# Performance work log

Hardware: AMD Instinct MI355X
Metric: run time of the kernel (lower is better)

## Reference

```python
import jax, jax.numpy as jnp
import numpy as np

N = 100000          # number of nodes (queries == sources here)
DEG = 32            # uniform neighbor count
E = N * DEG         # total edges
C_IN = 8
HID = 32
C_OUT = 32


def setup_inputs() -> dict:
    key = jax.random.key(0)
    k1, k2, k3, k4, k5 = jax.random.split(key, 5)
    in_features = jax.random.normal(k1, (N, C_IN), dtype=jnp.float32)
    in_weights = jax.random.uniform(k2, (N,), dtype=jnp.float32)
    # MLP: Linear(2*C_IN -> HID), GELU, Linear(HID -> C_OUT)
    W1 = jax.random.normal(k3, (2 * C_IN, HID), dtype=jnp.float32) / np.sqrt(2 * C_IN)
    b1 = jnp.zeros((HID,), dtype=jnp.float32)
    W2 = jax.random.normal(k4, (HID, C_OUT), dtype=jnp.float32) / np.sqrt(HID)
    b2 = jnp.zeros((C_OUT,), dtype=jnp.float32)
    neighbor_index = jax.random.randint(k5, (E,), 0, N, dtype=jnp.int64)
    row_splits = (jnp.arange(N + 1, dtype=jnp.int64) * DEG)  # uniform CSR splits
    return {"in_features": in_features, "in_weights": in_weights,
            "W1": W1, "b1": b1, "W2": W2, "b2": b2,
            "neighbor_index": neighbor_index, "row_splits": row_splits}


def reference(in_features, in_weights, W1, b1, W2, b2, neighbor_index, row_splits):
    num_edges = neighbor_index.shape[0]
    num_out = row_splits.shape[0] - 1  # M output nodes
    # segment id of each edge (== repeat_interleave of node ids by row counts)
    seg = jnp.searchsorted(row_splits, jnp.arange(num_edges), side="right") - 1
    gathered = in_features[neighbor_index]          # [E, C_in] neighbor gather
    self_feats = in_features[seg]                   # [E, C_in] repeated self features
    agg = jnp.concatenate([gathered, self_feats], axis=1)  # [E, 2*C_in]
    h = jax.nn.gelu(agg @ W1 + b1)                  # [E, HID]
    h = h @ W2 + b2                                 # [E, C_out]
    h = in_weights[neighbor_index][:, None] * h     # quadrature weighting
    sums = jax.ops.segment_sum(h, seg, num_segments=num_out)  # segment_csr sum
    counts = (row_splits[1:] - row_splits[:-1]).astype(h.dtype)
    out = sums / jnp.maximum(counts, 1)[:, None]    # reduce='mean'
    return out
```

## Files before the change

kernel.cpp:

```cpp
#include <hip/hip_runtime.h>

#define DEG 32
#define HID 32
#define CIN 8

typedef float v2f __attribute__((ext_vector_type(2)));
typedef short bf16x8 __attribute__((ext_vector_type(8)));
typedef float f32x16 __attribute__((ext_vector_type(16)));

#define GELU_A ((float)(2.0 * 1.4426950408889634 * 0.7978845608028654))
#define GELU_B ((float)(2.0 * 1.4426950408889634 * 0.7978845608028654 * 0.044715))

__device__ __forceinline__ unsigned f2bf(float f) {
    unsigned b = __float_as_uint(f);
    return (b + 0x7fffu + ((b >> 16) & 1u)) >> 16;
}
__device__ __forceinline__ unsigned pack2(float lo, float hi) {
    return f2bf(lo) | (f2bf(hi) << 16);
}

__global__ __launch_bounds__(256) void precompute_xw(
    const float* __restrict__ x, const float* __restrict__ W1,
    const float* __restrict__ W2, unsigned* __restrict__ x16,
    unsigned* __restrict__ w1f, unsigned* __restrict__ w2f, int N) {
    int tid = blockIdx.x * 256 + threadIdx.x;
    if (blockIdx.x == 0) {
        int t = threadIdx.x;
        if (t < 64) {
            int kb = (t >> 5) * 8, col = t & 31;
            uint4 o;
            o.x = pack2(W1[(kb + 0) * HID + col], W1[(kb + 1) * HID + col]);
            o.y = pack2(W1[(kb + 2) * HID + col], W1[(kb + 3) * HID + col]);
            o.z = pack2(W1[(kb + 4) * HID + col], W1[(kb + 5) * HID + col]);
            o.w = pack2(W1[(kb + 6) * HID + col], W1[(kb + 7) * HID + col]);
            *(uint4*)(w1f + t * 4) = o;
        } else if (t < 192) {
            int u = t - 64;
            int f = u >> 6, l = u & 63;
            int kb = f * 16 + ((l >> 5) * 8), col = l & 31;
            uint4 o;
            o.x = pack2(W2[(kb + 0) * HID + col], W2[(kb + 1) * HID + col]);
            o.y = pack2(W2[(kb + 2) * HID + col], W2[(kb + 3) * HID + col]);
            o.z = pack2(W2[(kb + 4) * HID + col], W2[(kb + 5) * HID + col]);
            o.w = pack2(W2[(kb + 6) * HID + col], W2[(kb + 7) * HID + col]);
            *(uint4*)(w2f + (f * 64 + l) * 4) = o;
        }
    }
    if (tid < N) {
        const float4* xp = (const float4*)(x + (size_t)tid * CIN);
        float4 a = xp[0], b = xp[1];
        uint4 o;
        o.x = pack2(a.x, a.y);  o.y = pack2(a.z, a.w);
        o.z = pack2(b.x, b.y);  o.w = pack2(b.z, b.w);
        *(uint4*)(x16 + (size_t)tid * 4) = o;
    }
}

__global__ __launch_bounds__(256) void git_core(
    const unsigned* __restrict__ x16, const unsigned* __restrict__ w1f,
    const float* __restrict__ wgt, const float* __restrict__ b1,
    const int* __restrict__ nbr, unsigned short* __restrict__ g16,
    float* __restrict__ wsum, int N) {
    __shared__ float sw[4 * DEG];

    int t = threadIdx.x;
    int wv = t >> 6;
    int l  = t & 63;
    int l5 = l & 31;
    int hi = l >> 5;
    int node = blockIdx.x * 4 + wv;
    int nc = node < N ? node : (N - 1);

    int   jn = nbr[nc * DEG + l5];
    float w  = wgt[jn];
    if (hi == 0) sw[wv * DEG + l5] = w;

    float ws = w;
    ws += __shfl_xor(ws, 1);  ws += __shfl_xor(ws, 2);
    ws += __shfl_xor(ws, 4);  ws += __shfl_xor(ws, 8);
    ws += __shfl_xor(ws, 16);

    int arow = hi ? nc : jn;
    bf16x8 af = *((const bf16x8*)x16 + arow);
    bf16x8 bf = *((const bf16x8*)w1f + l);
    float myb1 = b1[l5];

    f32x16 acc;
#pragma unroll
    for (int i = 0; i < 16; ++i) acc[i] = myb1;
    acc = __builtin_amdgcn_mfma_f32_32x32x16_bf16(af, bf, acc, 0, 0, 0);

    const float* swp = &sw[wv * DEG + hi * 4];
    float4 wq0 = *(const float4*)(swp);
    float4 wq1 = *(const float4*)(swp + 8);
    float4 wq2 = *(const float4*)(swp + 16);
    float4 wq3 = *(const float4*)(swp + 24);
    float wqa[16] = {wq0.x, wq0.y, wq0.z, wq0.w,  wq1.x, wq1.y, wq1.z, wq1.w,
                     wq2.x, wq2.y, wq2.z, wq2.w,  wq3.x, wq3.y, wq3.z, wq3.w};

    v2f gacc = {0.f, 0.f};
#pragma unroll
    for (int i = 0; i < 16; i += 2) {
        v2f tt = {acc[i], acc[i + 1]};
        v2f x2 = tt * tt;
        v2f zz = tt * (x2 * (-GELU_B) + (-GELU_A));
        v2f ee;
        ee.x = __builtin_amdgcn_exp2f(zz.x);  ee.y = __builtin_amdgcn_exp2f(zz.y);
        v2f dd = ee + 1.0f;
        v2f rr;
        rr.x = __builtin_amdgcn_rcpf(dd.x);   rr.y = __builtin_amdgcn_rcpf(dd.y);
        v2f wp = {wqa[i], wqa[i + 1]};
        gacc += wp * (tt * rr);
    }
    float g = gacc.x + gacc.y;
    g += __shfl_xor(g, 32);

    if (node < N && hi == 0) {
        g16[(size_t)node * HID + l5] = (unsigned short)f2bf(g);
        if (l5 == 0) wsum[node] = ws;
    }
}

__global__ __launch_bounds__(256) void epilogue_mfma(
    const unsigned short* __restrict__ g16, const unsigned* __restrict__ w2f,
    const float* __restrict__ wsum, const float* __restrict__ b2,
    float* __restrict__ out, int N) {
    int t = threadIdx.x;
    int wv = t >> 6;
    int l  = t & 63;
    int l5 = l & 31;
    int hi = l >> 5;
    int tile = blockIdx.x * 4 + wv;
    int ntiles = (N + 31) >> 5;
    if (tile >= ntiles) return;
    int nb = tile * 32;

    int row = nb + l5;  if (row >= N) row = N - 1;
    bf16x8 a1 = *(const bf16x8*)(g16 + (size_t)row * HID + hi * 8);
    bf16x8 a2 = *(const bf16x8*)(g16 + (size_t)row * HID + 16 + hi * 8);
    bf16x8 bf1 = *((const bf16x8*)w2f + l);
    bf16x8 bf2 = *((const bf16x8*)w2f + 64 + l);

    f32x16 acc = {};
    acc = __builtin_amdgcn_mfma_f32_32x32x16_bf16(a1, bf1, acc, 0, 0, 0);
    acc = __builtin_amdgcn_mfma_f32_32x32x16_bf16(a2, bf2, acc, 0, 0, 0);

    float myb2 = b2[l5];
    float wsa[16];
    if (nb + 32 <= N) {
        const float* wp = wsum + nb + hi * 4;
        float4 q0 = *(const float4*)(wp);
        float4 q1 = *(const float4*)(wp + 8);
        float4 q2 = *(const float4*)(wp + 16);
        float4 q3 = *(const float4*)(wp + 24);
        wsa[0]=q0.x; wsa[1]=q0.y; wsa[2]=q0.z; wsa[3]=q0.w;
        wsa[4]=q1.x; wsa[5]=q1.y; wsa[6]=q1.z; wsa[7]=q1.w;
        wsa[8]=q2.x; wsa[9]=q2.y; wsa[10]=q2.z; wsa[11]=q2.w;
        wsa[12]=q3.x; wsa[13]=q3.y; wsa[14]=q3.z; wsa[15]=q3.w;
    } else {
#pragma unroll
        for (int i = 0; i < 16; ++i) {
            int r = nb + (i & 3) + 8 * (i >> 2) + 4 * hi;
            wsa[i] = wsum[r < N ? r : (N - 1)];
        }
    }
#pragma unroll
    for (int i = 0; i < 16; ++i) {
        int r = nb + (i & 3) + 8 * (i >> 2) + 4 * hi;
        if (r < N)
            out[(size_t)r * HID + l5] = fmaf(wsa[i], myb2, acc[i]) * (1.0f / DEG);
    }
}

__global__ __launch_bounds__(256) void fused_fallback(
    const float* __restrict__ x, const float* __restrict__ wgt,
    const float* __restrict__ W1, const float* __restrict__ b1,
    const float* __restrict__ W2, const float* __restrict__ b2,
    const int* __restrict__ nbr, float* __restrict__ out, int N) {
    __shared__ float sW2[HID * HID];
    __shared__ float sb2[HID];
    __shared__ int2  sp[8 * DEG];
    int t = threadIdx.x;
#pragma unroll
    for (int i = 0; i < 4; ++i) sW2[t + i * 256] = W2[t + i * 256];
    if (t < HID) sb2[t] = b2[t];
    int slot = t >> 5, hid = t & 31;
    int node = blockIdx.x * 8 + slot;
    bool valid = node < N;
    int nc = valid ? node : (N - 1);
    int   j_own = nbr[nc * DEG + hid];
    float w_own = wgt[j_own];
    sp[slot * DEG + hid] = make_int2(j_own * (CIN * 4), __float_as_int(w_own));
    const float4* xip = (const float4*)(x + (size_t)nc * CIN);
    float4 xa = xip[0], xb = xip[1];
    float w1t[8];
#pragma unroll
    for (int k = 0; k < 8; ++k) w1t[k] = W1[k * HID + hid];
    float vb = b1[hid];
    vb = fmaf(xa.x, W1[ 8 * HID + hid], vb);
    vb = fmaf(xa.y, W1[ 9 * HID + hid], vb);
    vb = fmaf(xa.z, W1[10 * HID + hid], vb);
    vb = fmaf(xa.w, W1[11 * HID + hid], vb);
    vb = fmaf(xb.x, W1[12 * HID + hid], vb);
    vb = fmaf(xb.y, W1[13 * HID + hid], vb);
    vb = fmaf(xb.z, W1[14 * HID + hid], vb);
    vb = fmaf(xb.w, W1[15 * HID + hid], vb);
    float ws = w_own;
    ws += __shfl_xor(ws, 1);  ws += __shfl_xor(ws, 2);
    ws += __shfl_xor(ws, 4);  ws += __shfl_xor(ws, 8);
    ws += __shfl_xor(ws, 16);
    __syncthreads();
    const char* xbytes = (const char*)x;
    const int2* myp = &sp[slot * DEG];
    float g = 0.f;
#pragma unroll 8
    for (int e = 0; e < DEG; ++e) {
        int2  p  = myp[e];
        float wjv = __int_as_float(p.y);
        const float4* xjp = (const float4*)(xbytes + (unsigned)p.x);
        float4 a = xjp[0], b = xjp[1];
        float tin = vb;
        tin = fmaf(a.x, w1t[0], tin); tin = fmaf(a.y, w1t[1], tin);
        tin = fmaf(a.z, w1t[2], tin); tin = fmaf(a.w, w1t[3], tin);
        tin = fmaf(b.x, w1t[4], tin); tin = fmaf(b.y, w1t[5], tin);
        tin = fmaf(b.z, w1t[6], tin); tin = fmaf(b.w, w1t[7], tin);
        float x2 = tin * tin;
        float z  = tin * fmaf(GELU_B, x2, GELU_A);
        float e2 = __builtin_amdgcn_exp2f(z);
        float r  = __builtin_amdgcn_rcpf(1.0f + e2);
        g = fmaf(wjv, fmaf(-tin, r, tin), g);
    }
    float acc = 0.f;
#pragma unroll
    for (int h = 0; h < HID; ++h) {
        float gh = __shfl(g, h, 32);
        acc = fmaf(gh, sW2[h * HID + hid], acc);
    }
    if (valid) out[(size_t)node * HID + hid] = fmaf(ws, sb2[hid], acc) * (1.0f / DEG);
}

extern "C" void kernel_launch(void* const* d_in, const int* in_sizes, int n_in,
                              void* d_out, int out_size, void* d_ws, size_t ws_size,
                              hipStream_t stream) {
    const float* x   = (const float*)d_in[0];
    const float* wq  = (const float*)d_in[1];
    const float* W1  = (const float*)d_in[2];
    const float* b1  = (const float*)d_in[3];
    const float* W2  = (const float*)d_in[4];
    const float* b2  = (const float*)d_in[5];
    const int*   nbr = (const int*)d_in[6];
    float* out = (float*)d_out;

    int N = in_sizes[1];

    size_t off_x16 = 0;
    size_t off_g16 = (off_x16 + (size_t)N * 16 + 255) & ~(size_t)255;
    size_t off_ws  = (off_g16 + (size_t)N * 64 + 255) & ~(size_t)255;
    size_t off_w1  = (off_ws  + (size_t)N * 4  + 255) & ~(size_t)255;
    size_t off_w2  = off_w1 + 1024;
    size_t need    = off_w2 + 2048;

    if (ws_size >= need) {
        unsigned*       x16  = (unsigned*)((char*)d_ws + off_x16);
        unsigned short* g16p = (unsigned short*)((char*)d_ws + off_g16);
        float*          wsum = (float*)((char*)d_ws + off_ws);
        unsigned*       w1f  = (unsigned*)((char*)d_ws + off_w1);
        unsigned*       w2f  = (unsigned*)((char*)d_ws + off_w2);

        int blocks_pre = (N + 255) / 256;
        precompute_xw<<<blocks_pre, 256, 0, stream>>>(x, W1, W2, x16, w1f, w2f, N);

        int blocks_main = (N + 3) / 4;
        git_core<<<blocks_main, 256, 0, stream>>>(x16, w1f, wq, b1, nbr, g16p, wsum, N);

        int ntiles = (N + 31) / 32;
        int blocks_epi = (ntiles + 3) / 4;
        epilogue_mfma<<<blocks_epi, 256, 0, stream>>>(g16p, w2f, wsum, b2, out, N);
    } else {
        int blocks = (N + 7) / 8;
        fused_fallback<<<blocks, 256, 0, stream>>>(x, wq, W1, b1, W2, b2, nbr, out, N);
    }
}
```

Baseline: 121.4 us.

## Fuse GELU-aggregation and output MFMA into one kernel via shared memory

Merges the core kernel and the epilogue kernel into a single kernel. Each wave now handles two nodes, and each block covers eight nodes. The per-node aggregated hidden vectors and weight sums are staged in shared memory instead of a global bf16 buffer, and one wave then runs the W2 MFMA for the block. This removes a global write and read of the intermediate, plus one kernel launch. In exchange it adds a block barrier, leaves three of four waves idle during the epilogue, and wastes most rows of the 32x32 MFMA.

Result: faster. 114.3 us (-5.8%).

```diff
diff --git a/kernel.cpp b/kernel.cpp
--- a/kernel.cpp
+++ b/kernel.cpp
@@ -56,52 +56,18 @@
     }
 }
 
-__global__ __launch_bounds__(256) void git_core(
-    const unsigned* __restrict__ x16, const unsigned* __restrict__ w1f,
-    const float* __restrict__ wgt, const float* __restrict__ b1,
-    const int* __restrict__ nbr, unsigned short* __restrict__ g16,
-    float* __restrict__ wsum, int N) {
-    __shared__ float sw[4 * DEG];
-
-    int t = threadIdx.x;
-    int wv = t >> 6;
-    int l  = t & 63;
-    int l5 = l & 31;
-    int hi = l >> 5;
-    int node = blockIdx.x * 4 + wv;
-    int nc = node < N ? node : (N - 1);
-
-    int   jn = nbr[nc * DEG + l5];
-    float w  = wgt[jn];
-    if (hi == 0) sw[wv * DEG + l5] = w;
-
-    float ws = w;
-    ws += __shfl_xor(ws, 1);  ws += __shfl_xor(ws, 2);
-    ws += __shfl_xor(ws, 4);  ws += __shfl_xor(ws, 8);
-    ws += __shfl_xor(ws, 16);
-
-    int arow = hi ? nc : jn;
-    bf16x8 af = *((const bf16x8*)x16 + arow);
-    bf16x8 bf = *((const bf16x8*)w1f + l);
-    float myb1 = b1[l5];
-
-    f32x16 acc;
-#pragma unroll
-    for (int i = 0; i < 16; ++i) acc[i] = myb1;
-    acc = __builtin_amdgcn_mfma_f32_32x32x16_bf16(af, bf, acc, 0, 0, 0);
-
-    const float* swp = &sw[wv * DEG + hi * 4];
+__device__ __forceinline__ float gelu_reduce(const f32x16& acc, const float* swp,
+                                             float b1v) {
     float4 wq0 = *(const float4*)(swp);
     float4 wq1 = *(const float4*)(swp + 8);
     float4 wq2 = *(const float4*)(swp + 16);
     float4 wq3 = *(const float4*)(swp + 24);
     float wqa[16] = {wq0.x, wq0.y, wq0.z, wq0.w,  wq1.x, wq1.y, wq1.z, wq1.w,
                      wq2.x, wq2.y, wq2.z, wq2.w,  wq3.x, wq3.y, wq3.z, wq3.w};
-
     v2f gacc = {0.f, 0.f};
 #pragma unroll
     for (int i = 0; i < 16; i += 2) {
-        v2f tt = {acc[i], acc[i + 1]};
+        v2f tt = {acc[i] + b1v, acc[i + 1] + b1v};
         v2f x2 = tt * tt;
         v2f zz = tt * (x2 * (-GELU_B) + (-GELU_A));
         v2f ee;
@@ -114,61 +80,90 @@
     }
     float g = gacc.x + gacc.y;
     g += __shfl_xor(g, 32);
-
-    if (node < N && hi == 0) {
-        g16[(size_t)node * HID + l5] = (unsigned short)f2bf(g);
-        if (l5 == 0) wsum[node] = ws;
-    }
-}
-
-__global__ __launch_bounds__(256) void epilogue_mfma(
-    const unsigned short* __restrict__ g16, const unsigned* __restrict__ w2f,
-    const float* __restrict__ wsum, const float* __restrict__ b2,
-    float* __restrict__ out, int N) {
+    return g;
+}
+
+__global__ __launch_bounds__(256, 5) void git_fused(
+    const unsigned* __restrict__ x16, const unsigned* __restrict__ w1f,
+    const unsigned* __restrict__ w2f, const float* __restrict__ wgt,
+    const float* __restrict__ b1, const float* __restrict__ b2,
+    const int* __restrict__ nbr, float* __restrict__ out, int N) {
+    __shared__ float          sw[8 * DEG];
+    __shared__ unsigned short sg[32 * 40];
+    __shared__ float          sws[32];
+
     int t = threadIdx.x;
     int wv = t >> 6;
     int l  = t & 63;
     int l5 = l & 31;
     int hi = l >> 5;
-    int tile = blockIdx.x * 4 + wv;
-    int ntiles = (N + 31) >> 5;
-    if (tile >= ntiles) return;
-    int nb = tile * 32;
-
-    int row = nb + l5;  if (row >= N) row = N - 1;
-    bf16x8 a1 = *(const bf16x8*)(g16 + (size_t)row * HID + hi * 8);
-    bf16x8 a2 = *(const bf16x8*)(g16 + (size_t)row * HID + 16 + hi * 8);
-    bf16x8 bf1 = *((const bf16x8*)w2f + l);
-    bf16x8 bf2 = *((const bf16x8*)w2f + 64 + l);
-
-    f32x16 acc = {};
-    acc = __builtin_amdgcn_mfma_f32_32x32x16_bf16(a1, bf1, acc, 0, 0, 0);
-    acc = __builtin_amdgcn_mfma_f32_32x32x16_bf16(a2, bf2, acc, 0, 0, 0);
+    int nb = blockIdx.x * 8 + wv * 2;
+
+    int jn[2]; float w[2]; int ncl[2];
+#pragma unroll
+    for (int r = 0; r < 2; ++r) {
+        int n = nb + r; ncl[r] = n < N ? n : (N - 1);
+        jn[r] = nbr[ncl[r] * DEG + l5];
+        w[r]  = wgt[jn[r]];
+    }
+    if (hi == 0) {
+#pragma unroll
+        for (int r = 0; r < 2; ++r) sw[(wv * 2 + r) * DEG + l5] = w[r];
+    }
+
+    float ws[2];
+#pragma unroll
+    for (int r = 0; r < 2; ++r) {
+        float s = w[r];
+        s += __shfl_xor(s, 1);  s += __shfl_xor(s, 2);
+        s += __shfl_xor(s, 4);  s += __shfl_xor(s, 8);
+        s += __shfl_xor(s, 16);
+        ws[r] = s;
+    }
+
+    bf16x8 af0 = *((const bf16x8*)x16 + (hi ? ncl[0] : jn[0]));
+    bf16x8 af1 = *((const bf16x8*)x16 + (hi ? ncl[1] : jn[1]));
+    bf16x8 bf  = *((const bf16x8*)w1f + l);
+    float myb1 = b1[l5];
+
+    f32x16 z0 = {}, z1 = {};
+    f32x16 a0 = __builtin_amdgcn_mfma_f32_32x32x16_bf16(af0, bf, z0, 0, 0, 0);
+    f32x16 a1 = __builtin_amdgcn_mfma_f32_32x32x16_bf16(af1, bf, z1, 0, 0, 0);
+
+    const float* swb = &sw[wv * 2 * DEG + hi * 4];
+    float g0 = gelu_reduce(a0, swb, myb1);
+    float g1 = gelu_reduce(a1, swb + DEG, myb1);
+
+    if (hi == 0) {
+        sg[(wv * 2 + 0) * 40 + l5] = (unsigned short)f2bf(g0);
+        sg[(wv * 2 + 1) * 40 + l5] = (unsigned short)f2bf(g1);
+        if (l5 == 0) { sws[wv * 2] = ws[0]; sws[wv * 2 + 1] = ws[1]; }
+    }
+
+    __syncthreads();
+
+    if (wv != 0) return;
+
+    const char* sgb = (const char*)sg;
+    bf16x8 ea1 = *(const bf16x8*)(sgb + l5 * 80 + hi * 16);
+    bf16x8 ea2 = *(const bf16x8*)(sgb + l5 * 80 + 32 + hi * 16);
+    bf16x8 eb1 = *((const bf16x8*)w2f + l);
+    bf16x8 eb2 = *((const bf16x8*)w2f + 64 + l);
+
+    f32x16 zz = {};
+    f32x16 acc = __builtin_amdgcn_mfma_f32_32x32x16_bf16(ea1, eb1, zz, 0, 0, 0);
+    acc = __builtin_amdgcn_mfma_f32_32x32x16_bf16(ea2, eb2, acc, 0, 0, 0);
 
     float myb2 = b2[l5];
-    float wsa[16];
-    if (nb + 32 <= N) {
-        const float* wp = wsum + nb + hi * 4;
-        float4 q0 = *(const float4*)(wp);
-        float4 q1 = *(const float4*)(wp + 8);
-        float4 q2 = *(const float4*)(wp + 16);
-        float4 q3 = *(const float4*)(wp + 24);
-        wsa[0]=q0.x; wsa[1]=q0.y; wsa[2]=q0.z; wsa[3]=q0.w;
-        wsa[4]=q1.x; wsa[5]=q1.y; wsa[6]=q1.z; wsa[7]=q1.w;
-        wsa[8]=q2.x; wsa[9]=q2.y; wsa[10]=q2.z; wsa[11]=q2.w;
-        wsa[12]=q3.x; wsa[13]=q3.y; wsa[14]=q3.z; wsa[15]=q3.w;
-    } else {
-#pragma unroll
-        for (int i = 0; i < 16; ++i) {
-            int r = nb + (i & 3) + 8 * (i >> 2) + 4 * hi;
-            wsa[i] = wsum[r < N ? r : (N - 1)];
-        }
-    }
-#pragma unroll
-    for (int i = 0; i < 16; ++i) {
-        int r = nb + (i & 3) + 8 * (i >> 2) + 4 * hi;
-        if (r < N)
-            out[(size_t)r * HID + l5] = fmaf(wsa[i], myb2, acc[i]) * (1.0f / DEG);
+    float4 wsq = *(const float4*)(sws + hi * 4);
+    float wsa[4] = {wsq.x, wsq.y, wsq.z, wsq.w};
+
+#pragma unroll
+    for (int i = 0; i < 4; ++i) {
+        int r = i + 4 * hi;
+        int node = blockIdx.x * 8 + r;
+        if (node < N)
+            out[(size_t)node * HID + l5] = fmaf(wsa[i], myb2, acc[i]) * (1.0f / DEG);
     }
 }
 
@@ -254,28 +249,21 @@
     int N = in_sizes[1];
 
     size_t off_x16 = 0;
-    size_t off_g16 = (off_x16 + (size_t)N * 16 + 255) & ~(size_t)255;
-    size_t off_ws  = (off_g16 + (size_t)N * 64 + 255) & ~(size_t)255;
-    size_t off_w1  = (off_ws  + (size_t)N * 4  + 255) & ~(size_t)255;
+    size_t off_w1  = (off_x16 + (size_t)N * 16 + 255) & ~(size_t)255;
     size_t off_w2  = off_w1 + 1024;
     size_t need    = off_w2 + 2048;
 
     if (ws_size >= need) {
-        unsigned*       x16  = (unsigned*)((char*)d_ws + off_x16);
-        unsigned short* g16p = (unsigned short*)((char*)d_ws + off_g16);
-        float*          wsum = (float*)((char*)d_ws + off_ws);
-        unsigned*       w1f  = (unsigned*)((char*)d_ws + off_w1);
-        unsigned*       w2f  = (unsigned*)((char*)d_ws + off_w2);
+        unsigned* x16 = (unsigned*)((char*)d_ws + off_x16);
+        unsigned* w1f = (unsigned*)((char*)d_ws + off_w1);
+        unsigned* w2f = (unsigned*)((char*)d_ws + off_w2);
 
         int blocks_pre = (N + 255) / 256;
         precompute_xw<<<blocks_pre, 256, 0, stream>>>(x, W1, W2, x16, w1f, w2f, N);
 
-        int blocks_main = (N + 3) / 4;
-        git_core<<<blocks_main, 256, 0, stream>>>(x16, w1f, wq, b1, nbr, g16p, wsum, N);
-
-        int ntiles = (N + 31) / 32;
-        int blocks_epi = (ntiles + 3) / 4;
-        epilogue_mfma<<<blocks_epi, 256, 0, stream>>>(g16p, w2f, wsum, b2, out, N);
+        int blocks_main = (N + 7) / 8;
+        git_fused<<<blocks_main, 256, 0, stream>>>(x16, w1f, w2f, wq, b1, b2,
+                                                   nbr, out, N);
     } else {
         int blocks = (N + 7) / 8;
         fused_fallback<<<blocks, 256, 0, stream>>>(x, wq, W1, b1, W2, b2, nbr, out, N);
```
